# Kernel tuning notes

Hardware: AMD Instinct MI355X
Metric: run time of the kernel (lower is better)

The kernel has to match this reference:

```python
import jax, jax.numpy as jnp
import numpy as np

NS, NV = 32, 8                      # scalar / vector multiplicities (32x0e + 8x1o)
N_NODES, N_EDGES = 16384, 131072
NEF, HID = 128, 128                 # edge feature dim, MLP hidden
WN = NS*NS + NV*NS + NS*NV + NV*NV  # 1600 tensor-product weights per edge
D = NS + 3*NV                       # 56 node feature dim
INV_SQRT3 = 1.0/np.sqrt(3.0)        # CG coeff for 1o x 1o -> 0e
PATH_NORM = 1.0/np.sqrt(NS + NV)    # fan-in normalization per output irrep
EPS = 1e-5


def setup_inputs() -> dict:
    key = jax.random.key(0)
    ks = jax.random.split(key, 10)
    node_attr = jax.random.normal(ks[0], (N_NODES, D), jnp.float32)
    edge_index = jax.random.randint(ks[1], (2, N_EDGES), 0, N_NODES, dtype=jnp.int64)
    edge_attr = jax.random.normal(ks[2], (N_EDGES, NEF), jnp.float32)
    edge_sh = jax.random.normal(ks[3], (N_EDGES, 4), jnp.float32)
    W1 = jax.random.normal(ks[4], (NEF, HID), jnp.float32) / np.sqrt(NEF)
    b1 = jnp.zeros((HID,), jnp.float32)
    W2 = jax.random.normal(ks[5], (HID, WN), jnp.float32) / np.sqrt(HID)
    b2 = jnp.zeros((WN,), jnp.float32)
    bn_gamma = jnp.ones((NS + NV,), jnp.float32)   # per-irrep scale (scalars then vectors)
    bn_beta = jnp.zeros((NS,), jnp.float32)        # bias only on scalar irreps
    return dict(node_attr=node_attr, edge_attr=edge_attr, edge_sh=edge_sh,
                W1=W1, b1=b1, W2=W2, b2=b2, bn_gamma=bn_gamma, bn_beta=bn_beta,
                edge_index=edge_index)


def reference(node_attr, edge_attr, edge_sh, W1, b1, W2, b2, bn_gamma, bn_beta, edge_index):
    edge_src, edge_dst = edge_index[0], edge_index[1]

    # per-edge tensor-product weights from edge MLP (dropout=0, eval mode)
    w = jax.nn.relu(edge_attr @ W1 + b1) @ W2 + b2            # [E, WN]
    o0 = NS*NS; o1 = o0 + NV*NS; o2 = o1 + NS*NV
    w_ss = w[:, :o0].reshape(-1, NS, NS)   # 0e x 0e -> 0e
    w_vs = w[:, o0:o1].reshape(-1, NV, NS) # 1o x 1o -> 0e
    w_sv = w[:, o1:o2].reshape(-1, NS, NV) # 0e x 1o -> 1o
    w_vv = w[:, o2:].reshape(-1, NV, NV)   # 1o x 0e -> 1o

    # gather node features onto edges
    x = node_attr[edge_dst]                # [E, D]
    xs = x[:, :NS]                         # [E, NS]
    xv = x[:, NS:].reshape(-1, NV, 3)      # [E, NV, 3]
    ss = edge_sh[:, 0]                     # [E]
    sv = edge_sh[:, 1:4]                   # [E, 3]

    # CG tensor product with per-edge fully-connected weights
    dot_vv = jnp.einsum('eim,em->ei', xv, sv) * INV_SQRT3
    out_s = (jnp.einsum('eij,ei->ej', w_ss, xs) * ss[:, None]
             + jnp.einsum('eij,ei->ej', w_vs, dot_vv)) * PATH_NORM          # [E, NS]
    out_v = (jnp.einsum('eij,ei->ej', w_sv, xs)[:, :, None] * sv[:, None, :]
             + jnp.einsum('eij,eim->ejm', w_vv, xv) * ss[:, None, None]) * PATH_NORM  # [E, NV, 3]
    tp = jnp.concatenate([out_s, out_v.reshape(-1, 3*NV)], axis=-1)         # [E, D]

    # scatter-mean to source nodes
    sums = jax.ops.segment_sum(tp, edge_src, num_segments=N_NODES)
    cnt = jax.ops.segment_sum(jnp.ones((tp.shape[0], 1), tp.dtype), edge_src,
                              num_segments=N_NODES)
    out = sums / jnp.maximum(cnt, 1.0)

    # residual (in/out irreps identical -> zero padding is a no-op)
    out = out + node_attr

    # equivariant batch norm (training-mode batch statistics)
    s = out[:, :NS]
    v = out[:, NS:].reshape(-1, NV, 3)
    s = (s - s.mean(0)) / jnp.sqrt(s.var(0) + EPS) * bn_gamma[:NS] + bn_beta
    vn2 = (v * v).sum(-1).mean(0)                               # [NV] mean squared norm
    v = v / jnp.sqrt(vn2 + EPS)[None, :, None] * bn_gamma[NS:][None, :, None]
    return jnp.concatenate([s, v.reshape(-1, 3*NV)], axis=-1)
```

## Files before the change

kernel.cpp:

```cpp
#include <hip/hip_runtime.h>

typedef short short8 __attribute__((ext_vector_type(8)));
typedef unsigned short us4 __attribute__((ext_vector_type(4)));
typedef float floatx4 __attribute__((ext_vector_type(4)));
typedef unsigned short u16;

#define NN 16384
#define NE 131072
#define NEF_ 128
#define DD 56
#define INV_SQRT3F 0.57735026918962576f
#define PATH_NORMF 0.15811388300841897f

__device__ __forceinline__ float bf2f(u16 u) {
    union { unsigned int i; float f; } v; v.i = ((unsigned int)u) << 16; return v.f;
}
__device__ __forceinline__ u16 f2bf(float f) {
    union { float f; unsigned int i; } v; v.f = f;
    unsigned int r = v.i + 0x7fffu + ((v.i >> 16) & 1u);
    return (u16)(r >> 16);
}

__device__ __forceinline__ int sa_off(int row, int col) {
    return (row << 7) + (col ^ ((row & 7) << 3));
}

__global__ __launch_bounds__(256) void prep(const float* __restrict__ W1,
                                            const float* __restrict__ W2,
                                            u16* __restrict__ W1f,
                                            u16* __restrict__ W2f,
                                            const int* __restrict__ eidx,
                                            int* __restrict__ deg) {
    int b = blockIdx.x;
    if (b < 864) {
        int i = b * 256 + threadIdx.x;
        if (i < 16384) {
            int cc = i >> 13, kk = (i >> 11) & 3, cg = (i >> 9) & 3;
            int lane = (i >> 3) & 63, j = i & 7;
            int q = lane >> 4, m = lane & 15;
            W1f[i] = f2bf(W1[(kk * 32 + q * 8 + j) * 128 + cc * 64 + cg * 16 + m]);
        } else {
            int f = i - 16384;
            int c = f >> 13, kk = (f >> 11) & 3, cg = (f >> 9) & 3;
            int lane = (f >> 3) & 63, j = f & 7;
            int q = lane >> 4, m = lane & 15;
            W2f[f] = f2bf(W2[(kk * 32 + q * 8 + j) * 1600 + c * 64 + cg * 16 + m]);
        }
    } else {
        int e = (b - 864) * 256 + threadIdx.x;
        atomicAdd(&deg[eidx[e]], 1);
    }
}

__global__ __launch_bounds__(1024) void deg_scan(const int* __restrict__ deg,
                                                 int* __restrict__ row_start,
                                                 int* __restrict__ cursor) {
    __shared__ int part[1024];
    const int t = threadIdx.x;
    const int base = t * 16;
    int loc[16];
    int s = 0;
    #pragma unroll
    for (int i = 0; i < 16; i++) { loc[i] = s; s += deg[base + i]; }
    part[t] = s;
    __syncthreads();
    for (int off = 1; off < 1024; off <<= 1) {
        int v = (t >= off) ? part[t - off] : 0;
        __syncthreads();
        part[t] += v;
        __syncthreads();
    }
    int pre = (t == 0) ? 0 : part[t - 1];
    #pragma unroll
    for (int i = 0; i < 16; i++) {
        int v = pre + loc[i];
        row_start[base + i] = v;
        cursor[base + i] = v;
    }
    if (t == 1023) row_start[16384] = pre + s;
}

__global__ __launch_bounds__(256) void edge_scatter(const int* __restrict__ eidx,
                                                    int* __restrict__ cursor,
                                                    int* __restrict__ edge_order) {
    int e = blockIdx.x * 256 + threadIdx.x;
    int p = atomicAdd(&cursor[eidx[e]], 1);
    edge_order[p] = e;
}

__global__ __launch_bounds__(512, 4) void tpconv(
    const float* __restrict__ node_attr, const float* __restrict__ edge_attr,
    const float* __restrict__ edge_sh, const u16* __restrict__ W1f,
    const float* __restrict__ b1, const u16* __restrict__ W2f,
    const float* __restrict__ b2, const int* __restrict__ eidx,
    const int* __restrict__ edge_order,
    float* __restrict__ tp)
{
    __shared__ __align__(16) char smem[73728];
    u16*   sA  = (u16*)smem;
    u16*   sF  = (u16*)(smem + 32768);
    u16*   B2a = (u16*)(smem + 49152);
    u16*   B2b = (u16*)smem;
    float* b2s = (float*)(smem + 65536);
    float* Ssc  = (float*)smem;
    float* Svec = (float*)(smem + 33792);

    const int t = threadIdx.x;
    const int lane = t & 63;
    const int wv = t >> 6;
    const int m = lane & 15;
    const int q = lane >> 4;
    const int cg = wv & 1;
    const int ew = wv >> 1;
    const int p0 = blockIdx.x * 128;

    short8 pre[2];
    #pragma unroll
    for (int ii = 0; ii < 2; ii++)
        pre[ii] = *(const short8*)&W2f[ii * 4096 + t * 8];

    for (int i = t; i < 1600; i += 512) b2s[i] = b2[i];

    short8 g[4];
    #pragma unroll
    for (int kk = 0; kk < 4; kk++)
        g[kk] = *(const short8*)&W1f[(wv >> 2) * 8192 + (kk * 4 + (wv & 3)) * 512 + lane * 8];

    #pragma unroll
    for (int ii = 0; ii < 8; ii++) {
        int cid = t + 512 * ii;
        int r = cid >> 5, s = cid & 31;
        int e = edge_order[p0 + r];
        const float* src = &edge_attr[(size_t)e * NEF_ + s * 4];
        us4 o;
        o.x = f2bf(src[0]); o.y = f2bf(src[1]); o.z = f2bf(src[2]); o.w = f2bf(src[3]);
        *(us4*)&sA[sa_off(r, s * 4)] = o;
    }
    {
        int e = t & 127, p = t >> 7;
        int eg = edge_order[p0 + e];
        int nd = eidx[NE + eg];
        const float* na = node_attr + (size_t)nd * DD;
        if (p < 2) {
            #pragma unroll
            for (int k = 0; k < 16; k++)
                sF[(p * 16 + k) * 128 + e] = f2bf(na[p * 16 + k]);
        } else if (p == 2) {
            const float* sh = edge_sh + (size_t)eg * 4;
            float s0 = sh[1], s1 = sh[2], s2 = sh[3];
            #pragma unroll
            for (int i = 0; i < 8; i++) {
                float d = (na[32 + 3 * i] * s0 + na[33 + 3 * i] * s1 + na[34 + 3 * i] * s2) * INV_SQRT3F;
                sF[(32 + i) * 128 + e] = f2bf(d);
            }
        } else {
            #pragma unroll
            for (int k = 0; k < 24; k++)
                sF[(40 + k) * 128 + e] = f2bf(na[32 + k]);
        }
    }
    #pragma unroll
    for (int ii = 0; ii < 2; ii++)
        *(short8*)&B2a[ii * 4096 + t * 8] = pre[ii];
    #pragma unroll
    for (int ii = 0; ii < 2; ii++)
        pre[ii] = *(const short8*)&W2f[8192 + ii * 4096 + t * 8];
    __syncthreads();

    floatx4 hacc[8];
    {
        float bv = b1[wv * 16 + m];
        #pragma unroll
        for (int rt = 0; rt < 8; rt++) hacc[rt] = (floatx4){bv, bv, bv, bv};
    }
    #pragma unroll
    for (int kk = 0; kk < 4; kk++)
        #pragma unroll
        for (int rt = 0; rt < 8; rt++) {
            short8 a = *(const short8*)&sA[sa_off(rt * 16 + m, kk * 32 + q * 8)];
            hacc[rt] = __builtin_amdgcn_mfma_f32_16x16x32_bf16(a, g[kk], hacc[rt], 0, 0, 0);
        }
    __syncthreads();
    #pragma unroll
    for (int rt = 0; rt < 8; rt++)
        #pragma unroll
        for (int r = 0; r < 4; r++) {
            int e = rt * 16 + q * 4 + r;
            float v = hacc[rt][r];
            sA[sa_off(e, wv * 16 + m)] = f2bf(v > 0.f ? v : 0.f);
        }
    __syncthreads();

    const int e0 = ew * 32 + m;
    const int e1 = ew * 32 + 16 + m;
    short8 hc[2][4];
    #pragma unroll
    for (int et = 0; et < 2; et++)
        #pragma unroll
        for (int kk = 0; kk < 4; kk++)
            hc[et][kk] = *(const short8*)&sA[sa_off(ew * 32 + et * 16 + m, kk * 32 + q * 8)];

    float ssc[2], svc[2][3];
    #pragma unroll
    for (int et = 0; et < 2; et++) {
        int eg = edge_order[p0 + ew * 32 + et * 16 + m];
        const float* sh = edge_sh + (size_t)eg * 4;
        ssc[et] = sh[0]; svc[et][0] = sh[1]; svc[et][1] = sh[2]; svc[et][2] = sh[3];
    }
    __syncthreads();

    float tps[2][2][4];
    float tpv[2][4][3];
    #pragma unroll
    for (int et = 0; et < 2; et++)
        #pragma unroll
        for (int r = 0; r < 4; r++) {
            tps[et][0][r] = 0.f; tps[et][1][r] = 0.f;
            tpv[et][r][0] = 0.f; tpv[et][r][1] = 0.f; tpv[et][r][2] = 0.f;
        }

    for (int c = 0; c < 25; c++) {
        const u16* rb = (c & 1) ? B2b : B2a;
        u16*       wb = (c & 1) ? B2a : B2b;

        floatx4 acc[2][2];
        #pragma unroll
        for (int ct = 0; ct < 2; ct++) {
            floatx4 bias = *(const floatx4*)&b2s[c * 64 + cg * 32 + ct * 16 + q * 4];
            acc[ct][0] = bias; acc[ct][1] = bias;
        }
        #pragma unroll
        for (int kk = 0; kk < 4; kk++)
            #pragma unroll
            for (int ct = 0; ct < 2; ct++) {
                short8 a = *(const short8*)&rb[(kk * 4 + cg * 2 + ct) * 512 + lane * 8];
                acc[ct][0] = __builtin_amdgcn_mfma_f32_16x16x32_bf16(a, hc[0][kk], acc[ct][0], 0, 0, 0);
                acc[ct][1] = __builtin_amdgcn_mfma_f32_16x16x32_bf16(a, hc[1][kk], acc[ct][1], 0, 0, 0);
            }

        if (c < 24) {
            #pragma unroll
            for (int ii = 0; ii < 2; ii++)
                *(short8*)&wb[ii * 4096 + t * 8] = pre[ii];
            if (c < 23) {
                #pragma unroll
                for (int ii = 0; ii < 2; ii++)
                    pre[ii] = *(const short8*)&W2f[(size_t)(c + 2) * 8192 + ii * 4096 + t * 8];
            }
        }

        if (c < 16) {
            const int i = 2 * c + cg;
            #pragma unroll
            for (int et = 0; et < 2; et++) {
                float f = bf2f(sF[i * 128 + (et ? e1 : e0)]) * ssc[et];
                #pragma unroll
                for (int ct = 0; ct < 2; ct++)
                    #pragma unroll
                    for (int r = 0; r < 4; r++) tps[et][ct][r] += acc[ct][et][r] * f;
            }
        } else if (c < 20) {
            const int i = 2 * (c - 16) + cg;
            #pragma unroll
            for (int et = 0; et < 2; et++) {
                float f = bf2f(sF[(32 + i) * 128 + (et ? e1 : e0)]);
                #pragma unroll
                for (int ct = 0; ct < 2; ct++)
                    #pragma unroll
                    for (int r = 0; r < 4; r++) tps[et][ct][r] += acc[ct][et][r] * f;
            }
        } else if (c < 24) {
            #pragma unroll
            for (int ct = 0; ct < 2; ct++) {
                const int i = 8 * (c - 20) + cg * 4 + ct * 2 + (q >> 1);
                #pragma unroll
                for (int et = 0; et < 2; et++) {
                    float f = bf2f(sF[i * 128 + (et ? e1 : e0)]);
                    #pragma unroll
                    for (int r = 0; r < 4; r++) {
                        float t0 = acc[ct][et][r] * f;
                        tpv[et][r][0] += t0 * svc[et][0];
                        tpv[et][r][1] += t0 * svc[et][1];
                        tpv[et][r][2] += t0 * svc[et][2];
                    }
                }
            }
        } else {
            #pragma unroll
            for (int ct = 0; ct < 2; ct++) {
                const int i = cg * 4 + ct * 2 + (q >> 1);
                #pragma unroll
                for (int et = 0; et < 2; et++) {
                    const int ee = et ? e1 : e0;
                    float x0 = bf2f(sF[(40 + 3 * i    ) * 128 + ee]) * ssc[et];
                    float x1 = bf2f(sF[(40 + 3 * i + 1) * 128 + ee]) * ssc[et];
                    float x2 = bf2f(sF[(40 + 3 * i + 2) * 128 + ee]) * ssc[et];
                    #pragma unroll
                    for (int r = 0; r < 4; r++) {
                        tpv[et][r][0] += acc[ct][et][r] * x0;
                        tpv[et][r][1] += acc[ct][et][r] * x1;
                        tpv[et][r][2] += acc[ct][et][r] * x2;
                    }
                }
            }
        }

        __syncthreads();
    }

    #pragma unroll
    for (int et = 0; et < 2; et++) {
        const int ee = et ? e1 : e0;
        #pragma unroll
        for (int ct = 0; ct < 2; ct++)
            #pragma unroll
            for (int r = 0; r < 4; r++)
                Ssc[(cg * 128 + ee) * 33 + ct * 16 + q * 4 + r] = tps[et][ct][r];
    }
    #pragma unroll
    for (int et = 0; et < 2; et++) {
        const int ee = et ? e1 : e0;
        #pragma unroll
        for (int r = 0; r < 4; r++)
            #pragma unroll
            for (int mm = 0; mm < 3; mm++) {
                float v = tpv[et][r][mm];
                v += __shfl_xor(v, 32, 64);
                if (q < 2)
                    Svec[(cg * 128 + ee) * 25 + (q * 4 + r) * 3 + mm] = v;
            }
    }
    __syncthreads();

    for (int idx = t; idx < 7168; idx += 512) {
        int e = idx / 56, d = idx - e * 56;
        float v;
        if (d < 32) {
            v = Ssc[e * 33 + d] + Ssc[(128 + e) * 33 + d];
        } else {
            int dd = d - 32;
            v = Svec[e * 25 + dd] + Svec[(128 + e) * 25 + dd];
        }
        tp[(size_t)(p0 + e) * DD + d] = v * PATH_NORMF;
    }
}

__global__ __launch_bounds__(256) void gather_finalize(
    const float* __restrict__ tp, const int* __restrict__ row_start,
    const float* __restrict__ node_attr,
    float* __restrict__ ybuf, float* __restrict__ partial)
{
    __shared__ float ps[4][72];
    const int wv = threadIdx.x >> 6, lane = threadIdx.x & 63;
    const int n = blockIdx.x * 4 + wv;
    const int beg = row_start[n], end = row_start[n + 1];
    if (lane < 56) {
        float acc = 0.f;
        for (int p = beg; p < end; p++)
            acc += tp[(size_t)p * DD + lane];
        float inv = 1.f / fmaxf((float)(end - beg), 1.f);
        float y = acc * inv + node_attr[(size_t)n * DD + lane];
        ybuf[(size_t)n * DD + lane] = y;
        if (lane < 32) {
            ps[wv][lane] = y;
            ps[wv][32 + lane] = y * y;
        } else {
            float vv = y * y;
            float v1 = __shfl_down(vv, 1, 64);
            float v2 = __shfl_down(vv, 2, 64);
            int l3 = lane - 32;
            if (l3 % 3 == 0) ps[wv][64 + l3 / 3] = vv + v1 + v2;
        }
    }
    __syncthreads();
    const int t = threadIdx.x;
    if (t < 72)
        partial[(size_t)blockIdx.x * 72 + t] = ps[0][t] + ps[1][t] + ps[2][t] + ps[3][t];
}

__global__ __launch_bounds__(256) void bn_reduce(const float* __restrict__ partial,
                                                 float* __restrict__ stats)
{
    __shared__ float red[256];
    const int d = blockIdx.x;
    const int t = threadIdx.x;
    float a = 0.f;
    for (int i = t; i < 4096; i += 256) a += partial[(size_t)i * 72 + d];
    red[t] = a;
    __syncthreads();
    for (int off = 128; off > 0; off >>= 1) {
        if (t < off) red[t] += red[t + off];
        __syncthreads();
    }
    if (t == 0) stats[d] = red[0] * (1.f / 16384.f);
}

__global__ __launch_bounds__(256) void bn_apply(
    const float* __restrict__ ybuf, const float* __restrict__ stats,
    const float* __restrict__ gamma, const float* __restrict__ beta,
    float* __restrict__ out)
{
    const int i = blockIdx.x * 256 + threadIdx.x;
    const int n = i / 56;
    const int d = i - n * 56;
    float y = ybuf[i];
    float o;
    if (d < 32) {
        float mn  = stats[d];
        float var = stats[32 + d] - mn * mn;
        o = (y - mn) * rsqrtf(var + 1e-5f) * gamma[d] + beta[d];
    } else {
        int jv = (d - 32) / 3;
        o = y * rsqrtf(stats[64 + jv] + 1e-5f) * gamma[32 + jv];
    }
    out[i] = o;
}

extern "C" void kernel_launch(void* const* d_in, const int* in_sizes, int n_in,
                              void* d_out, int out_size, void* d_ws, size_t ws_size,
                              hipStream_t stream)
{
    const float* node_attr = (const float*)d_in[0];
    const float* edge_attr = (const float*)d_in[1];
    const float* edge_sh   = (const float*)d_in[2];
    const float* W1        = (const float*)d_in[3];
    const float* b1        = (const float*)d_in[4];
    const float* W2        = (const float*)d_in[5];
    const float* b2        = (const float*)d_in[6];
    const float* gamma     = (const float*)d_in[7];
    const float* beta      = (const float*)d_in[8];
    const int*   eidx      = (const int*)d_in[9];

    char* ws = (char*)d_ws;
    u16*   W1f        = (u16*)(ws);
    u16*   W2f        = (u16*)(ws + 32768);
    int*   deg        = (int*)(ws + 442368);
    int*   row_start  = (int*)(ws + 507904);
    int*   cursor     = (int*)(ws + 573696);
    int*   edge_order = (int*)(ws + 639232);
    float* stats      = (float*)(ws + 1163520);
    float* partial    = (float*)(ws + 1164032);
    float* tp         = (float*)(ws + 2343680);
    float* ybuf       = (float*)(ws + 31703808);

    (void)hipMemsetAsync(deg, 0, 65536, stream);
    hipLaunchKernelGGL(prep,            dim3(1376), dim3(256),  0, stream,
                       W1, W2, W1f, W2f, eidx, deg);
    hipLaunchKernelGGL(deg_scan,        dim3(1),    dim3(1024), 0, stream, deg, row_start, cursor);
    hipLaunchKernelGGL(edge_scatter,    dim3(512),  dim3(256),  0, stream, eidx, cursor, edge_order);
    hipLaunchKernelGGL(tpconv,          dim3(1024), dim3(512),  0, stream,
                       node_attr, edge_attr, edge_sh, W1f, b1, W2f, b2, eidx, edge_order, tp);
    hipLaunchKernelGGL(gather_finalize, dim3(4096), dim3(256),  0, stream,
                       tp, row_start, node_attr, ybuf, partial);
    hipLaunchKernelGGL(bn_reduce,       dim3(72),   dim3(256),  0, stream, partial, stats);
    hipLaunchKernelGGL(bn_apply,        dim3(3584), dim3(256),  0, stream,
                       ybuf, stats, gamma, beta, (float*)d_out);
}
```

Measured before the change: 254.3 us.

## Replace CSR sort-and-gather with direct atomic scatter into node sums

Removes the degree scan and edge-scatter kernels that built a source-sorted edge order, and the per-edge tp buffer written to global memory. The tpconv kernel now walks edges in natural order and accumulates results straight into a zeroed per-node sums buffer with float atomicAdd, while finalize divides by the degree counts. This drops two kernel launches, the indirect edge_order lookups, and a 29 MB intermediate write and read. In exchange it issues about 7M global float atomics with random contention, and the summation order becomes nondeterministic.

```diff
diff --git a/kernel.cpp b/kernel.cpp
--- a/kernel.cpp
+++ b/kernel.cpp
@@ -52,49 +52,12 @@
     }
 }
 
-__global__ __launch_bounds__(1024) void deg_scan(const int* __restrict__ deg,
-                                                 int* __restrict__ row_start,
-                                                 int* __restrict__ cursor) {
-    __shared__ int part[1024];
-    const int t = threadIdx.x;
-    const int base = t * 16;
-    int loc[16];
-    int s = 0;
-    #pragma unroll
-    for (int i = 0; i < 16; i++) { loc[i] = s; s += deg[base + i]; }
-    part[t] = s;
-    __syncthreads();
-    for (int off = 1; off < 1024; off <<= 1) {
-        int v = (t >= off) ? part[t - off] : 0;
-        __syncthreads();
-        part[t] += v;
-        __syncthreads();
-    }
-    int pre = (t == 0) ? 0 : part[t - 1];
-    #pragma unroll
-    for (int i = 0; i < 16; i++) {
-        int v = pre + loc[i];
-        row_start[base + i] = v;
-        cursor[base + i] = v;
-    }
-    if (t == 1023) row_start[16384] = pre + s;
-}
-
-__global__ __launch_bounds__(256) void edge_scatter(const int* __restrict__ eidx,
-                                                    int* __restrict__ cursor,
-                                                    int* __restrict__ edge_order) {
-    int e = blockIdx.x * 256 + threadIdx.x;
-    int p = atomicAdd(&cursor[eidx[e]], 1);
-    edge_order[p] = e;
-}
-
 __global__ __launch_bounds__(512, 4) void tpconv(
     const float* __restrict__ node_attr, const float* __restrict__ edge_attr,
     const float* __restrict__ edge_sh, const u16* __restrict__ W1f,
     const float* __restrict__ b1, const u16* __restrict__ W2f,
     const float* __restrict__ b2, const int* __restrict__ eidx,
-    const int* __restrict__ edge_order,
-    float* __restrict__ tp)
+    float* __restrict__ sums)
 {
     __shared__ __align__(16) char smem[73728];
     u16*   sA  = (u16*)smem;
@@ -102,8 +65,6 @@
     u16*   B2a = (u16*)(smem + 49152);
     u16*   B2b = (u16*)smem;
     float* b2s = (float*)(smem + 65536);
-    float* Ssc  = (float*)smem;
-    float* Svec = (float*)(smem + 33792);
 
     const int t = threadIdx.x;
     const int lane = t & 63;
@@ -130,15 +91,14 @@
     for (int ii = 0; ii < 8; ii++) {
         int cid = t + 512 * ii;
         int r = cid >> 5, s = cid & 31;
-        int e = edge_order[p0 + r];
-        const float* src = &edge_attr[(size_t)e * NEF_ + s * 4];
+        const float* src = &edge_attr[(size_t)(p0 + r) * NEF_ + s * 4];
         us4 o;
         o.x = f2bf(src[0]); o.y = f2bf(src[1]); o.z = f2bf(src[2]); o.w = f2bf(src[3]);
         *(us4*)&sA[sa_off(r, s * 4)] = o;
     }
     {
         int e = t & 127, p = t >> 7;
-        int eg = edge_order[p0 + e];
+        int eg = p0 + e;
         int nd = eidx[NE + eg];
         const float* na = node_attr + (size_t)nd * DD;
         if (p < 2) {
@@ -203,8 +163,7 @@
     float ssc[2], svc[2][3];
     #pragma unroll
     for (int et = 0; et < 2; et++) {
-        int eg = edge_order[p0 + ew * 32 + et * 16 + m];
-        const float* sh = edge_sh + (size_t)eg * 4;
+        const float* sh = edge_sh + (size_t)(p0 + ew * 32 + et * 16 + m) * 4;
         ssc[et] = sh[0]; svc[et][0] = sh[1]; svc[et][1] = sh[2]; svc[et][2] = sh[3];
     }
     __syncthreads();
@@ -308,58 +267,47 @@
         __syncthreads();
     }
 
-    #pragma unroll
-    for (int et = 0; et < 2; et++) {
-        const int ee = et ? e1 : e0;
+    {
+        const int ns0 = eidx[p0 + e0];
+        const int ns1 = eidx[p0 + e1];
+        float* s0p = sums + (size_t)ns0 * DD;
+        float* s1p = sums + (size_t)ns1 * DD;
         #pragma unroll
         for (int ct = 0; ct < 2; ct++)
             #pragma unroll
-            for (int r = 0; r < 4; r++)
-                Ssc[(cg * 128 + ee) * 33 + ct * 16 + q * 4 + r] = tps[et][ct][r];
-    }
-    #pragma unroll
-    for (int et = 0; et < 2; et++) {
-        const int ee = et ? e1 : e0;
+            for (int r = 0; r < 4; r++) {
+                int j = ct * 16 + q * 4 + r;
+                atomicAdd(&s0p[j], tps[0][ct][r] * PATH_NORMF);
+                atomicAdd(&s1p[j], tps[1][ct][r] * PATH_NORMF);
+            }
         #pragma unroll
         for (int r = 0; r < 4; r++)
             #pragma unroll
             for (int mm = 0; mm < 3; mm++) {
-                float v = tpv[et][r][mm];
-                v += __shfl_xor(v, 32, 64);
-                if (q < 2)
-                    Svec[(cg * 128 + ee) * 25 + (q * 4 + r) * 3 + mm] = v;
-            }
-    }
-    __syncthreads();
-
-    for (int idx = t; idx < 7168; idx += 512) {
-        int e = idx / 56, d = idx - e * 56;
-        float v;
-        if (d < 32) {
-            v = Ssc[e * 33 + d] + Ssc[(128 + e) * 33 + d];
-        } else {
-            int dd = d - 32;
-            v = Svec[e * 25 + dd] + Svec[(128 + e) * 25 + dd];
-        }
-        tp[(size_t)(p0 + e) * DD + d] = v * PATH_NORMF;
-    }
-}
-
-__global__ __launch_bounds__(256) void gather_finalize(
-    const float* __restrict__ tp, const int* __restrict__ row_start,
+                float v0 = tpv[0][r][mm];
+                v0 += __shfl_xor(v0, 32, 64);
+                float v1 = tpv[1][r][mm];
+                v1 += __shfl_xor(v1, 32, 64);
+                if (q < 2) {
+                    int d = 32 + (q * 4 + r) * 3 + mm;
+                    atomicAdd(&s0p[d], v0 * PATH_NORMF);
+                    atomicAdd(&s1p[d], v1 * PATH_NORMF);
+                }
+            }
+    }
+}
+
+__global__ __launch_bounds__(256) void node_finalize(
+    const float* __restrict__ sums, const int* __restrict__ deg,
     const float* __restrict__ node_attr,
     float* __restrict__ ybuf, float* __restrict__ partial)
 {
     __shared__ float ps[4][72];
     const int wv = threadIdx.x >> 6, lane = threadIdx.x & 63;
     const int n = blockIdx.x * 4 + wv;
-    const int beg = row_start[n], end = row_start[n + 1];
     if (lane < 56) {
-        float acc = 0.f;
-        for (int p = beg; p < end; p++)
-            acc += tp[(size_t)p * DD + lane];
-        float inv = 1.f / fmaxf((float)(end - beg), 1.f);
-        float y = acc * inv + node_attr[(size_t)n * DD + lane];
+        float inv = 1.f / fmaxf((float)deg[n], 1.f);
+        float y = sums[(size_t)n * DD + lane] * inv + node_attr[(size_t)n * DD + lane];
         ybuf[(size_t)n * DD + lane] = y;
         if (lane < 32) {
             ps[wv][lane] = y;
@@ -432,27 +380,22 @@
     const int*   eidx      = (const int*)d_in[9];
 
     char* ws = (char*)d_ws;
-    u16*   W1f        = (u16*)(ws);
-    u16*   W2f        = (u16*)(ws + 32768);
-    int*   deg        = (int*)(ws + 442368);
-    int*   row_start  = (int*)(ws + 507904);
-    int*   cursor     = (int*)(ws + 573696);
-    int*   edge_order = (int*)(ws + 639232);
-    float* stats      = (float*)(ws + 1163520);
-    float* partial    = (float*)(ws + 1164032);
-    float* tp         = (float*)(ws + 2343680);
-    float* ybuf       = (float*)(ws + 31703808);
-
-    (void)hipMemsetAsync(deg, 0, 65536, stream);
-    hipLaunchKernelGGL(prep,            dim3(1376), dim3(256),  0, stream,
+    u16*   W1f     = (u16*)(ws);
+    u16*   W2f     = (u16*)(ws + 32768);
+    int*   deg     = (int*)(ws + 442368);
+    float* sums    = (float*)(ws + 507904);
+    float* stats   = (float*)(ws + 4177920);
+    float* partial = (float*)(ws + 4178432);
+    float* ybuf    = (float*)(ws + 5358080);
+
+    (void)hipMemsetAsync(ws + 442368, 0, 3735552, stream);
+    hipLaunchKernelGGL(prep,          dim3(1376), dim3(256), 0, stream,
                        W1, W2, W1f, W2f, eidx, deg);
-    hipLaunchKernelGGL(deg_scan,        dim3(1),    dim3(1024), 0, stream, deg, row_start, cursor);
-    hipLaunchKernelGGL(edge_scatter,    dim3(512),  dim3(256),  0, stream, eidx, cursor, edge_order);
-    hipLaunchKernelGGL(tpconv,          dim3(1024), dim3(512),  0, stream,
-                       node_attr, edge_attr, edge_sh, W1f, b1, W2f, b2, eidx, edge_order, tp);
-    hipLaunchKernelGGL(gather_finalize, dim3(4096), dim3(256),  0, stream,
-                       tp, row_start, node_attr, ybuf, partial);
-    hipLaunchKernelGGL(bn_reduce,       dim3(72),   dim3(256),  0, stream, partial, stats);
-    hipLaunchKernelGGL(bn_apply,        dim3(3584), dim3(256),  0, stream,
+    hipLaunchKernelGGL(tpconv,        dim3(1024), dim3(512), 0, stream,
+                       node_attr, edge_attr, edge_sh, W1f, b1, W2f, b2, eidx, sums);
+    hipLaunchKernelGGL(node_finalize, dim3(4096), dim3(256), 0, stream,
+                       sums, deg, node_attr, ybuf, partial);
+    hipLaunchKernelGGL(bn_reduce,     dim3(72),   dim3(256), 0, stream, partial, stats);
+    hipLaunchKernelGGL(bn_apply,      dim3(3584), dim3(256), 0, stream,
                        ybuf, stats, gamma, beta, (float*)d_out);
 }
```

Result: slower. 601.8 us (+136.7%).

## Fuse CSR prep and BN tail into cooperative kernels with grid syncs

Applied to the files above, without the earlier changes.

Merges the weight-format conversion, degree count, scan and edge scatter into one cooperative kernel that uses grid-wide syncs. The gather, batch-norm reduction and apply steps become a second cooperative kernel that keeps node outputs in registers, so the intermediate ybuf round trip through global memory goes away. This replaces six launches with two and drops a large intermediate buffer. In exchange it adds grid.sync costs, requires all 1024 blocks to be co-resident, and performs the scan with a single-thread loop per block.

```diff
diff --git a/kernel.cpp b/kernel.cpp
--- a/kernel.cpp
+++ b/kernel.cpp
@@ -1,4 +1,7 @@
 #include <hip/hip_runtime.h>
+#include <hip/hip_cooperative_groups.h>
+
+namespace cg = cooperative_groups;
 
 typedef short short8 __attribute__((ext_vector_type(8)));
 typedef unsigned short us4 __attribute__((ext_vector_type(4)));
@@ -25,67 +28,73 @@
     return (row << 7) + (col ^ ((row & 7) << 3));
 }
 
-__global__ __launch_bounds__(256) void prep(const float* __restrict__ W1,
-                                            const float* __restrict__ W2,
-                                            u16* __restrict__ W1f,
-                                            u16* __restrict__ W2f,
-                                            const int* __restrict__ eidx,
-                                            int* __restrict__ deg) {
-    int b = blockIdx.x;
-    if (b < 864) {
-        int i = b * 256 + threadIdx.x;
-        if (i < 16384) {
-            int cc = i >> 13, kk = (i >> 11) & 3, cg = (i >> 9) & 3;
-            int lane = (i >> 3) & 63, j = i & 7;
-            int q = lane >> 4, m = lane & 15;
-            W1f[i] = f2bf(W1[(kk * 32 + q * 8 + j) * 128 + cc * 64 + cg * 16 + m]);
-        } else {
-            int f = i - 16384;
-            int c = f >> 13, kk = (f >> 11) & 3, cg = (f >> 9) & 3;
-            int lane = (f >> 3) & 63, j = f & 7;
-            int q = lane >> 4, m = lane & 15;
-            W2f[f] = f2bf(W2[(kk * 32 + q * 8 + j) * 1600 + c * 64 + cg * 16 + m]);
-        }
-    } else {
-        int e = (b - 864) * 256 + threadIdx.x;
-        atomicAdd(&deg[eidx[e]], 1);
-    }
-}
-
-__global__ __launch_bounds__(1024) void deg_scan(const int* __restrict__ deg,
-                                                 int* __restrict__ row_start,
-                                                 int* __restrict__ cursor) {
-    __shared__ int part[1024];
-    const int t = threadIdx.x;
-    const int base = t * 16;
-    int loc[16];
-    int s = 0;
-    #pragma unroll
-    for (int i = 0; i < 16; i++) { loc[i] = s; s += deg[base + i]; }
-    part[t] = s;
-    __syncthreads();
-    for (int off = 1; off < 1024; off <<= 1) {
-        int v = (t >= off) ? part[t - off] : 0;
+__global__ __launch_bounds__(256) void csr_prep(
+    const float* __restrict__ W1, const float* __restrict__ W2,
+    u16* __restrict__ W1f, u16* __restrict__ W2f,
+    const int* __restrict__ eidx, int* __restrict__ deg,
+    int* __restrict__ row_start, int* __restrict__ cursor,
+    int* __restrict__ edge_order, int* __restrict__ bsum, int* __restrict__ ebsum)
+{
+    cg::grid_group grid = cg::this_grid();
+    __shared__ int sloc[16];
+    __shared__ int sscan[256];
+    const int b = blockIdx.x, t = threadIdx.x;
+    const int gid = b * 256 + t;
+
+    if (gid < 16384) {
+        int i = gid;
+        int cc = i >> 13, kk = (i >> 11) & 3, cg4 = (i >> 9) & 3;
+        int lane = (i >> 3) & 63, j = i & 7;
+        int q = lane >> 4, m = lane & 15;
+        W1f[i] = f2bf(W1[(kk * 32 + q * 8 + j) * 128 + cc * 64 + cg4 * 16 + m]);
+    } else if (gid < 221184) {
+        int f = gid - 16384;
+        int c = f >> 13, kk = (f >> 11) & 3, cg4 = (f >> 9) & 3;
+        int lane = (f >> 3) & 63, j = f & 7;
+        int q = lane >> 4, m = lane & 15;
+        W2f[f] = f2bf(W2[(kk * 32 + q * 8 + j) * 1600 + c * 64 + cg4 * 16 + m]);
+    }
+    if (gid < NE) atomicAdd(&deg[eidx[gid]], 1);
+    grid.sync();
+
+    if (t == 0) {
+        int s = 0;
+        #pragma unroll
+        for (int i = 0; i < 16; i++) { sloc[i] = s; s += deg[b * 16 + i]; }
+        bsum[b] = s;
+    }
+    grid.sync();
+
+    if (b == 0) {
+        int v[4]; int s4 = 0;
+        #pragma unroll
+        for (int i = 0; i < 4; i++) { v[i] = bsum[t * 4 + i]; s4 += v[i]; }
+        sscan[t] = s4;
         __syncthreads();
-        part[t] += v;
-        __syncthreads();
-    }
-    int pre = (t == 0) ? 0 : part[t - 1];
-    #pragma unroll
-    for (int i = 0; i < 16; i++) {
-        int v = pre + loc[i];
-        row_start[base + i] = v;
-        cursor[base + i] = v;
-    }
-    if (t == 1023) row_start[16384] = pre + s;
-}
-
-__global__ __launch_bounds__(256) void edge_scatter(const int* __restrict__ eidx,
-                                                    int* __restrict__ cursor,
-                                                    int* __restrict__ edge_order) {
-    int e = blockIdx.x * 256 + threadIdx.x;
-    int p = atomicAdd(&cursor[eidx[e]], 1);
-    edge_order[p] = e;
+        for (int off = 1; off < 256; off <<= 1) {
+            int x = (t >= off) ? sscan[t - off] : 0;
+            __syncthreads();
+            sscan[t] += x;
+            __syncthreads();
+        }
+        int run = (t == 0) ? 0 : sscan[t - 1];
+        #pragma unroll
+        for (int i = 0; i < 4; i++) { ebsum[t * 4 + i] = run; run += v[i]; }
+        if (t == 255) row_start[16384] = sscan[255];
+    }
+    grid.sync();
+
+    if (t < 16) {
+        int v = ebsum[b] + sloc[t];
+        row_start[b * 16 + t] = v;
+        cursor[b * 16 + t] = v;
+    }
+    grid.sync();
+
+    if (gid < NE) {
+        int p = atomicAdd(&cursor[eidx[gid]], 1);
+        edge_order[p] = gid;
+    }
 }
 
 __global__ __launch_bounds__(512, 4) void tpconv(
@@ -110,7 +119,7 @@
     const int wv = t >> 6;
     const int m = lane & 15;
     const int q = lane >> 4;
-    const int cg = wv & 1;
+    const int cg4 = wv & 1;
     const int ew = wv >> 1;
     const int p0 = blockIdx.x * 128;
 
@@ -226,14 +235,14 @@
         floatx4 acc[2][2];
         #pragma unroll
         for (int ct = 0; ct < 2; ct++) {
-            floatx4 bias = *(const floatx4*)&b2s[c * 64 + cg * 32 + ct * 16 + q * 4];
+            floatx4 bias = *(const floatx4*)&b2s[c * 64 + cg4 * 32 + ct * 16 + q * 4];
             acc[ct][0] = bias; acc[ct][1] = bias;
         }
         #pragma unroll
         for (int kk = 0; kk < 4; kk++)
             #pragma unroll
             for (int ct = 0; ct < 2; ct++) {
-                short8 a = *(const short8*)&rb[(kk * 4 + cg * 2 + ct) * 512 + lane * 8];
+                short8 a = *(const short8*)&rb[(kk * 4 + cg4 * 2 + ct) * 512 + lane * 8];
                 acc[ct][0] = __builtin_amdgcn_mfma_f32_16x16x32_bf16(a, hc[0][kk], acc[ct][0], 0, 0, 0);
                 acc[ct][1] = __builtin_amdgcn_mfma_f32_16x16x32_bf16(a, hc[1][kk], acc[ct][1], 0, 0, 0);
             }
@@ -250,7 +259,7 @@
         }
 
         if (c < 16) {
-            const int i = 2 * c + cg;
+            const int i = 2 * c + cg4;
             #pragma unroll
             for (int et = 0; et < 2; et++) {
                 float f = bf2f(sF[i * 128 + (et ? e1 : e0)]) * ssc[et];
@@ -260,7 +269,7 @@
                     for (int r = 0; r < 4; r++) tps[et][ct][r] += acc[ct][et][r] * f;
             }
         } else if (c < 20) {
-            const int i = 2 * (c - 16) + cg;
+            const int i = 2 * (c - 16) + cg4;
             #pragma unroll
             for (int et = 0; et < 2; et++) {
                 float f = bf2f(sF[(32 + i) * 128 + (et ? e1 : e0)]);
@@ -272,7 +281,7 @@
         } else if (c < 24) {
             #pragma unroll
             for (int ct = 0; ct < 2; ct++) {
-                const int i = 8 * (c - 20) + cg * 4 + ct * 2 + (q >> 1);
+                const int i = 8 * (c - 20) + cg4 * 4 + ct * 2 + (q >> 1);
                 #pragma unroll
                 for (int et = 0; et < 2; et++) {
                     float f = bf2f(sF[i * 128 + (et ? e1 : e0)]);
@@ -288,7 +297,7 @@
         } else {
             #pragma unroll
             for (int ct = 0; ct < 2; ct++) {
-                const int i = cg * 4 + ct * 2 + (q >> 1);
+                const int i = cg4 * 4 + ct * 2 + (q >> 1);
                 #pragma unroll
                 for (int et = 0; et < 2; et++) {
                     const int ee = et ? e1 : e0;
@@ -315,7 +324,7 @@
         for (int ct = 0; ct < 2; ct++)
             #pragma unroll
             for (int r = 0; r < 4; r++)
-                Ssc[(cg * 128 + ee) * 33 + ct * 16 + q * 4 + r] = tps[et][ct][r];
+                Ssc[(cg4 * 128 + ee) * 33 + ct * 16 + q * 4 + r] = tps[et][ct][r];
     }
     #pragma unroll
     for (int et = 0; et < 2; et++) {
@@ -327,7 +336,7 @@
                 float v = tpv[et][r][mm];
                 v += __shfl_xor(v, 32, 64);
                 if (q < 2)
-                    Svec[(cg * 128 + ee) * 25 + (q * 4 + r) * 3 + mm] = v;
+                    Svec[(cg4 * 128 + ee) * 25 + (q * 4 + r) * 3 + mm] = v;
             }
     }
     __syncthreads();
@@ -345,75 +354,81 @@
     }
 }
 
-__global__ __launch_bounds__(256) void gather_finalize(
+__global__ __launch_bounds__(256) void tail_bn(
     const float* __restrict__ tp, const int* __restrict__ row_start,
-    const float* __restrict__ node_attr,
-    float* __restrict__ ybuf, float* __restrict__ partial)
+    const float* __restrict__ node_attr, const float* __restrict__ gamma,
+    const float* __restrict__ beta, float* __restrict__ partial,
+    float* __restrict__ stats, float* __restrict__ out)
 {
+    cg::grid_group grid = cg::this_grid();
     __shared__ float ps[4][72];
-    const int wv = threadIdx.x >> 6, lane = threadIdx.x & 63;
-    const int n = blockIdx.x * 4 + wv;
-    const int beg = row_start[n], end = row_start[n + 1];
-    if (lane < 56) {
-        float acc = 0.f;
-        for (int p = beg; p < end; p++)
-            acc += tp[(size_t)p * DD + lane];
-        float inv = 1.f / fmaxf((float)(end - beg), 1.f);
-        float y = acc * inv + node_attr[(size_t)n * DD + lane];
-        ybuf[(size_t)n * DD + lane] = y;
-        if (lane < 32) {
-            ps[wv][lane] = y;
-            ps[wv][32 + lane] = y * y;
-        } else {
-            float vv = y * y;
-            float v1 = __shfl_down(vv, 1, 64);
-            float v2 = __shfl_down(vv, 2, 64);
-            int l3 = lane - 32;
-            if (l3 % 3 == 0) ps[wv][64 + l3 / 3] = vv + v1 + v2;
-        }
-    }
-    __syncthreads();
-    const int t = threadIdx.x;
-    if (t < 72)
-        partial[(size_t)blockIdx.x * 72 + t] = ps[0][t] + ps[1][t] + ps[2][t] + ps[3][t];
-}
-
-__global__ __launch_bounds__(256) void bn_reduce(const float* __restrict__ partial,
-                                                 float* __restrict__ stats)
-{
     __shared__ float red[256];
-    const int d = blockIdx.x;
-    const int t = threadIdx.x;
-    float a = 0.f;
-    for (int i = t; i < 4096; i += 256) a += partial[(size_t)i * 72 + d];
-    red[t] = a;
-    __syncthreads();
-    for (int off = 128; off > 0; off >>= 1) {
-        if (t < off) red[t] += red[t + off];
+    const int b = blockIdx.x, t = threadIdx.x;
+    const int wv = t >> 6, lane = t & 63;
+
+    float yreg[4];
+    float acc72 = 0.f;
+
+    #pragma unroll
+    for (int pp = 0; pp < 4; pp++) {
+        const int n = b * 16 + pp * 4 + wv;
+        if (lane < 56) {
+            const int beg = row_start[n], end = row_start[n + 1];
+            float acc = 0.f;
+            for (int p = beg; p < end; p++)
+                acc += tp[(size_t)p * DD + lane];
+            float inv = 1.f / fmaxf((float)(end - beg), 1.f);
+            float y = acc * inv + node_attr[(size_t)n * DD + lane];
+            yreg[pp] = y;
+            if (lane < 32) {
+                ps[wv][lane] = y;
+                ps[wv][32 + lane] = y * y;
+            } else {
+                float vv = y * y;
+                float v1 = __shfl_down(vv, 1, 64);
+                float v2 = __shfl_down(vv, 2, 64);
+                int l3 = lane - 32;
+                if (l3 % 3 == 0) ps[wv][64 + l3 / 3] = vv + v1 + v2;
+            }
+        }
         __syncthreads();
-    }
-    if (t == 0) stats[d] = red[0] * (1.f / 16384.f);
-}
-
-__global__ __launch_bounds__(256) void bn_apply(
-    const float* __restrict__ ybuf, const float* __restrict__ stats,
-    const float* __restrict__ gamma, const float* __restrict__ beta,
-    float* __restrict__ out)
-{
-    const int i = blockIdx.x * 256 + threadIdx.x;
-    const int n = i / 56;
-    const int d = i - n * 56;
-    float y = ybuf[i];
-    float o;
-    if (d < 32) {
-        float mn  = stats[d];
-        float var = stats[32 + d] - mn * mn;
-        o = (y - mn) * rsqrtf(var + 1e-5f) * gamma[d] + beta[d];
-    } else {
-        int jv = (d - 32) / 3;
-        o = y * rsqrtf(stats[64 + jv] + 1e-5f) * gamma[32 + jv];
-    }
-    out[i] = o;
+        if (t < 72) acc72 += ps[0][t] + ps[1][t] + ps[2][t] + ps[3][t];
+        __syncthreads();
+    }
+    if (t < 72) partial[(size_t)b * 72 + t] = acc72;
+    grid.sync();
+
+    if (b < 72) {
+        float a = 0.f;
+        for (int i = t; i < 1024; i += 256) a += partial[(size_t)i * 72 + b];
+        red[t] = a;
+        __syncthreads();
+        for (int off = 128; off > 0; off >>= 1) {
+            if (t < off) red[t] += red[t + off];
+            __syncthreads();
+        }
+        if (t == 0) stats[b] = red[0] * (1.f / 16384.f);
+    }
+    grid.sync();
+
+    #pragma unroll
+    for (int pp = 0; pp < 4; pp++) {
+        const int n = b * 16 + pp * 4 + wv;
+        if (lane < 56) {
+            float y = yreg[pp];
+            int d = lane;
+            float o;
+            if (d < 32) {
+                float mn  = stats[d];
+                float var = stats[32 + d] - mn * mn;
+                o = (y - mn) * rsqrtf(var + 1e-5f) * gamma[d] + beta[d];
+            } else {
+                int jv = (d - 32) / 3;
+                o = y * rsqrtf(stats[64 + jv] + 1e-5f) * gamma[32 + jv];
+            }
+            out[(size_t)n * DD + d] = o;
+        }
+    }
 }
 
 extern "C" void kernel_launch(void* const* d_in, const int* in_sizes, int n_in,
@@ -430,6 +445,7 @@
     const float* gamma     = (const float*)d_in[7];
     const float* beta      = (const float*)d_in[8];
     const int*   eidx      = (const int*)d_in[9];
+    float*       out       = (float*)d_out;
 
     char* ws = (char*)d_ws;
     u16*   W1f        = (u16*)(ws);
@@ -438,21 +454,31 @@
     int*   row_start  = (int*)(ws + 507904);
     int*   cursor     = (int*)(ws + 573696);
     int*   edge_order = (int*)(ws + 639232);
-    float* stats      = (float*)(ws + 1163520);
-    float* partial    = (float*)(ws + 1164032);
-    float* tp         = (float*)(ws + 2343680);
-    float* ybuf       = (float*)(ws + 31703808);
+    int*   bsum       = (int*)(ws + 1163520);
+    int*   ebsum      = (int*)(ws + 1167616);
+    float* stats      = (float*)(ws + 1171712);
+    float* partial    = (float*)(ws + 1172224);
+    float* tp         = (float*)(ws + 1467136);
 
     (void)hipMemsetAsync(deg, 0, 65536, stream);
-    hipLaunchKernelGGL(prep,            dim3(1376), dim3(256),  0, stream,
-                       W1, W2, W1f, W2f, eidx, deg);
-    hipLaunchKernelGGL(deg_scan,        dim3(1),    dim3(1024), 0, stream, deg, row_start, cursor);
-    hipLaunchKernelGGL(edge_scatter,    dim3(512),  dim3(256),  0, stream, eidx, cursor, edge_order);
-    hipLaunchKernelGGL(tpconv,          dim3(1024), dim3(512),  0, stream,
-                       node_attr, edge_attr, edge_sh, W1f, b1, W2f, b2, eidx, edge_order, tp);
-    hipLaunchKernelGGL(gather_finalize, dim3(4096), dim3(256),  0, stream,
-                       tp, row_start, node_attr, ybuf, partial);
-    hipLaunchKernelGGL(bn_reduce,       dim3(72),   dim3(256),  0, stream, partial, stats);
-    hipLaunchKernelGGL(bn_apply,        dim3(3584), dim3(256),  0, stream,
-                       ybuf, stats, gamma, beta, (float*)d_out);
-}
+
+    {
+        void* args[] = {(void*)&W1, (void*)&W2, (void*)&W1f, (void*)&W2f,
+                        (void*)&eidx, (void*)&deg, (void*)&row_start, (void*)&cursor,
+                        (void*)&edge_order, (void*)&bsum, (void*)&ebsum};
+        (void)hipLaunchCooperativeKernel((void*)csr_prep, dim3(1024), dim3(256),
+                                         args, 0, stream);
+    }
+
+    hipLaunchKernelGGL(tpconv, dim3(1024), dim3(512), 0, stream,
+                       node_attr, edge_attr, edge_sh, W1f, b1, W2f, b2,
+                       eidx, edge_order, tp);
+
+    {
+        void* args[] = {(void*)&tp, (void*)&row_start, (void*)&node_attr,
+                        (void*)&gamma, (void*)&beta, (void*)&partial,
+                        (void*)&stats, (void*)&out};
+        (void)hipLaunchCooperativeKernel((void*)tail_bn, dim3(1024), dim3(256),
+                                         args, 0, stream);
+    }
+}
```

Result: slower. 868.9 us (+241.7%).
